# Kernel tuning notes

Hardware: AMD Instinct MI355X
Metric: run time of the kernel (lower is better)

The kernel has to match this reference:

```python
import jax, jax.numpy as jnp
import numpy as np

DECAY = 0.99
K = 8192
DIM = 512


def setup_inputs() -> dict:
    key = jax.random.key(0)
    k1, k2 = jax.random.split(key)
    z = jax.random.normal(k1, (8, 4096, DIM), dtype=jnp.float32)
    codebook = jax.random.normal(k2, (K, DIM), dtype=jnp.float32) * 0.02
    ema_count = jnp.zeros((K,), dtype=jnp.float32)
    ema_sum = jnp.zeros((K, DIM), dtype=jnp.float32)
    return {"z": z, "codebook": codebook, "ema_count": ema_count, "ema_sum": ema_sum}


def reference(z, codebook, ema_count, ema_sum):
    B, S, D = z.shape
    k = codebook.shape[0]
    z_flat = z.reshape(-1, D)  # [N, D]

    # squared euclidean distance: ||z||^2 + ||c||^2 - 2 z.c  -> [N, k]
    z2 = jnp.sum(z_flat * z_flat, axis=1, keepdims=True)
    c2 = jnp.sum(codebook * codebook, axis=1)
    logits = z_flat @ codebook.T
    dist = z2 + c2[None, :] - 2.0 * logits
    indices = jnp.argmin(dist, axis=1)  # [N]

    z_q = codebook[indices].reshape(z.shape)
    z_q_st = z + jax.lax.stop_gradient(z_q - z)  # straight-through

    loss_commit = jnp.mean((jax.lax.stop_gradient(z_q) - z) ** 2)
    loss_embed = jnp.mean((z_q - jax.lax.stop_gradient(z)) ** 2)

    # usage histogram (bincount), normalized
    ones = jnp.ones_like(indices, dtype=z.dtype)
    counts = jax.ops.segment_sum(ones, indices, num_segments=k)
    total = jnp.sum(counts)
    usage = jnp.where(total > 0, counts / total, counts)

    # EMA update (training-mode buffer update, all detached)
    zf = jax.lax.stop_gradient(z_flat)
    sums = jax.ops.segment_sum(zf, indices, num_segments=k)  # index_add
    new_ema_count = ema_count * DECAY + counts * (1.0 - DECAY)
    new_ema_sum = ema_sum * DECAY + sums * (1.0 - DECAY)
    denom = jnp.clip(new_ema_count[:, None], 1.0, None)
    new_codebook = new_ema_sum / denom

    return (z_q_st, indices.reshape(B, S), loss_commit, loss_embed, usage,
            new_codebook, new_ema_count, new_ema_sum)
```

## Files before the change

kernel.cpp:

```cpp
#include <hip/hip_runtime.h>


#define DIMC 512
#define NTOK 32768
#define KCB  8192

#define OFF_IDX   16777216UL
#define OFF_LC    16809984UL
#define OFF_LE    16809985UL
#define OFF_USAGE 16809986UL
#define OFF_NCB   16818178UL
#define OFF_NEC   21012482UL
#define OFF_NES   21020674UL

typedef unsigned short u16;
typedef unsigned int u32;
typedef __attribute__((ext_vector_type(8))) short short8;
typedef __attribute__((ext_vector_type(8))) u16 ushort8;
typedef __attribute__((ext_vector_type(4))) float f32x4;

__device__ __forceinline__ u16 f2bf(float x) {
  u32 u = __float_as_uint(x);
  return (u16)((u + 0x7fffu + ((u >> 16) & 1u)) >> 16);
}
__device__ __forceinline__ float bf2f(u16 h) { return __uint_as_float(((u32)h) << 16); }

#define GLL16(g, l) __builtin_amdgcn_global_load_lds( \
    (const __attribute__((address_space(1))) u32*)(g), \
    (__attribute__((address_space(3))) u32*)(l), 16, 0, 0)

__global__ __launch_bounds__(256)
void conv_norms(const float* __restrict__ z, const float* __restrict__ cb,
                u16* __restrict__ zh, u16* __restrict__ zl,
                u16* __restrict__ ch, u16* __restrict__ cl,
                float* __restrict__ z2, float* __restrict__ c2) {
  const int gid = blockIdx.x * 256 + threadIdx.x;
  const int lane = threadIdx.x & 63;
  int t = gid >> 6;
  const int g = gid & 63;
  const float* src; u16 *dh, *dl; float* nrm;
  if (t < NTOK) { src = z; dh = zh; dl = zl; nrm = z2; }
  else { t -= NTOK; src = cb; dh = ch; dl = cl; nrm = c2; }
  const float* p = src + (size_t)t * DIMC + g * 8;
  float4 v0 = *(const float4*)p;
  float4 v1 = *(const float4*)(p + 4);
  float in[8] = {v0.x, v0.y, v0.z, v0.w, v1.x, v1.y, v1.z, v1.w};
  ushort8 h, l;
  float ss = 0.f;
#pragma unroll
  for (int j = 0; j < 8; ++j) {
    ss += in[j] * in[j];
    u16 hb = f2bf(in[j]);
    h[j] = hb;
    l[j] = f2bf(in[j] - bf2f(hb));
  }
  const int mt = t >> 7, r = t & 127, ks = g >> 2, s = g & 3;
  const int sp = s ^ ((r >> 1) & 3);
  const size_t base = ((((size_t)mt * 16 + ks) * 128 + r) * 4 + sp) * 8;
  *(ushort8*)&dh[base] = h;
  *(ushort8*)&dl[base] = l;
#pragma unroll
  for (int off = 32; off; off >>= 1) ss += __shfl_down(ss, off);
  if (lane == 0) nrm[t] = ss;
}

__global__ __launch_bounds__(256)
void initkeys(unsigned long long* __restrict__ keys, double* __restrict__ loss) {
  const int i = blockIdx.x * 256 + threadIdx.x;
  keys[i] = 0xFFFFFFFFFFFFFFFFull;
  if (i == 0) *loss = 0.0;
}

__global__ __launch_bounds__(256)
void argmin_kernel(const u16* __restrict__ zh, const u16* __restrict__ zl,
                   const u16* __restrict__ ch, const u16* __restrict__ cl,
                   const float* __restrict__ z2, const float* __restrict__ c2,
                   unsigned long long* __restrict__ keys) {
  __shared__ __align__(16) char lds[32768];
  const int tid = threadIdx.x;
  const int mt = blockIdx.x, nt = blockIdx.y;
  const int lane = tid & 63;
  const int wid = tid >> 6;
  const int wr = wid >> 1, wn = wid & 1;
  const int lg = lane >> 4, lr = lane & 15;

  f32x4 acc[4][4];
#pragma unroll
  for (int m = 0; m < 4; ++m)
#pragma unroll
    for (int n = 0; n < 4; ++n) acc[m][n] = (f32x4)(0.f);

  const size_t abase = (size_t)mt * (16 * 4096);
  const size_t bbase = (size_t)nt * (16 * 4096);
  char* const la  = lds;
  char* const lal = lds + 8192;
  char* const lb  = lds + 16384;
  char* const lbl = lds + 24576;
  const int wlds = wid * 1024;
  const int goff = tid * 8;

  int aoff[4], boff[4];
#pragma unroll
  for (int m = 0; m < 4; ++m) {
    const int r = wr * 64 + m * 16 + lr;
    aoff[m] = r * 64 + ((lg ^ ((r >> 1) & 3)) * 16);
  }
#pragma unroll
  for (int n = 0; n < 4; ++n) {
    const int c = wn * 64 + n * 16 + lr;
    boff[n] = c * 64 + ((lg ^ ((c >> 1) & 3)) * 16);
  }

  for (int ks = 0; ks < 16; ++ks) {
    const size_t ao = abase + ks * 4096;
    const size_t bo = bbase + ks * 4096;
    __syncthreads();
    GLL16(zh + ao + goff,        la  + wlds);
    GLL16(zh + ao + 2048 + goff, la  + 4096 + wlds);
    GLL16(zl + ao + goff,        lal + wlds);
    GLL16(zl + ao + 2048 + goff, lal + 4096 + wlds);
    GLL16(ch + bo + goff,        lb  + wlds);
    GLL16(ch + bo + 2048 + goff, lb  + 4096 + wlds);
    GLL16(cl + bo + goff,        lbl + wlds);
    GLL16(cl + bo + 2048 + goff, lbl + 4096 + wlds);
    __syncthreads();
    short8 ah[4], alo[4], bh[4], blo[4];
#pragma unroll
    for (int m = 0; m < 4; ++m) {
      ah[m]  = *(const short8*)(la  + aoff[m]);
      alo[m] = *(const short8*)(lal + aoff[m]);
    }
#pragma unroll
    for (int n = 0; n < 4; ++n) {
      bh[n]  = *(const short8*)(lb  + boff[n]);
      blo[n] = *(const short8*)(lbl + boff[n]);
    }
#pragma unroll
    for (int m = 0; m < 4; ++m)
#pragma unroll
      for (int n = 0; n < 4; ++n) {
        acc[m][n] = __builtin_amdgcn_mfma_f32_16x16x32_bf16(alo[m], bh[n],  acc[m][n], 0, 0, 0);
        acc[m][n] = __builtin_amdgcn_mfma_f32_16x16x32_bf16(ah[m],  blo[n], acc[m][n], 0, 0, 0);
        acc[m][n] = __builtin_amdgcn_mfma_f32_16x16x32_bf16(ah[m],  bh[n],  acc[m][n], 0, 0, 0);
      }
  }

  const int row0 = mt * 128 + wr * 64;
  const int col0 = nt * 128 + wn * 64;
  float z2r[4][4];
#pragma unroll
  for (int m = 0; m < 4; ++m)
#pragma unroll
    for (int q = 0; q < 4; ++q)
      z2r[m][q] = z2[row0 + m * 16 + lg * 4 + q];
  float bv[4][4]; int bi[4][4];
#pragma unroll
  for (int m = 0; m < 4; ++m)
#pragma unroll
    for (int q = 0; q < 4; ++q) { bv[m][q] = 3.4e38f; bi[m][q] = 0x7fffffff; }
#pragma unroll
  for (int n = 0; n < 4; ++n) {
    const int cc = col0 + n * 16 + lr;
    const float c2v = c2[cc];
#pragma unroll
    for (int m = 0; m < 4; ++m)
#pragma unroll
      for (int q = 0; q < 4; ++q) {
        const float d = fmaf(-2.f, acc[m][n][q], z2r[m][q] + c2v);
        if (d < bv[m][q]) { bv[m][q] = d; bi[m][q] = cc; }
      }
  }
#pragma unroll
  for (int off = 1; off < 16; off <<= 1) {
#pragma unroll
    for (int m = 0; m < 4; ++m)
#pragma unroll
      for (int q = 0; q < 4; ++q) {
        const float ov = __shfl_xor(bv[m][q], off);
        const int oi = __shfl_xor(bi[m][q], off);
        if (ov < bv[m][q] || (ov == bv[m][q] && oi < bi[m][q])) { bv[m][q] = ov; bi[m][q] = oi; }
      }
  }
  if (lr == 0) {
#pragma unroll
    for (int m = 0; m < 4; ++m)
#pragma unroll
      for (int q = 0; q < 4; ++q) {
        const int token = row0 + m * 16 + lg * 4 + q;
        const unsigned long long pk =
            ((unsigned long long)__float_as_uint(bv[m][q]) << 32) | (u32)bi[m][q];
        atomicMin(&keys[token], pk);
      }
  }
}

__global__ __launch_bounds__(256)
void zero_kernel(float* __restrict__ usage_counts, float* __restrict__ sums) {
  const int gid = blockIdx.x * 256 + threadIdx.x;
  float2 zz; zz.x = 0.f; zz.y = 0.f;
  ((float2*)sums)[gid] = zz;
  ((float2*)sums)[gid + 1048576] = zz;
  if (gid < KCB) usage_counts[gid] = 0.f;
}

__global__ __launch_bounds__(128)
void gather_kernel(const float* __restrict__ z, const float* __restrict__ cb,
                   const unsigned long long* __restrict__ keys,
                   float* __restrict__ out, float* __restrict__ counts_acc,
                   float* __restrict__ sums_acc, double* __restrict__ loss_acc) {
  const int token = blockIdx.x;
  const int tid = threadIdx.x;
  const int idx = (int)(u32)(keys[token] & 0xFFFFFFFFull);
  if (tid == 0) {
    out[OFF_IDX + token] = (float)idx;
    unsafeAtomicAdd(&counts_acc[idx], 1.0f);
  }
  const float4 zv = *(const float4*)&z[(size_t)token * DIMC + tid * 4];
  const float4 cv = *(const float4*)&cb[(size_t)idx * DIMC + tid * 4];
  float4 o;
  o.x = zv.x + (cv.x - zv.x);
  o.y = zv.y + (cv.y - zv.y);
  o.z = zv.z + (cv.z - zv.z);
  o.w = zv.w + (cv.w - zv.w);
  *(float4*)&out[(size_t)token * DIMC + tid * 4] = o;
  const float ex = cv.x - zv.x, ey = cv.y - zv.y, ez = cv.z - zv.z, ew = cv.w - zv.w;
  float lsum = ex * ex; lsum += ey * ey; lsum += ez * ez; lsum += ew * ew;
  float* sp = &sums_acc[(size_t)idx * DIMC + tid * 4];
  unsafeAtomicAdd(sp + 0, zv.x);
  unsafeAtomicAdd(sp + 1, zv.y);
  unsafeAtomicAdd(sp + 2, zv.z);
  unsafeAtomicAdd(sp + 3, zv.w);
#pragma unroll
  for (int off = 32; off; off >>= 1) lsum += __shfl_down(lsum, off);
  if ((tid & 63) == 0) unsafeAtomicAdd(loss_acc, (double)lsum);
}

__global__ __launch_bounds__(256)
void finalize_mat(const float* __restrict__ ema_sum_in, const float* __restrict__ ema_cnt_in,
                  const float* __restrict__ counts_raw, float* __restrict__ nes,
                  float* __restrict__ ncb) {
  const int i2 = blockIdx.x * 256 + threadIdx.x;
  const size_t base = (size_t)i2 * 2;
  const int k = i2 >> 8;
  const float c = counts_raw[k];
  const float ncnt = ema_cnt_in[k] * 0.99f + c * 0.01f;
  const float denom = fmaxf(ncnt, 1.0f);
  float2 s = *(float2*)&nes[base];
  float2 e = *(const float2*)&ema_sum_in[base];
  float2 ns; ns.x = e.x * 0.99f + s.x * 0.01f; ns.y = e.y * 0.99f + s.y * 0.01f;
  *(float2*)&nes[base] = ns;
  float2 q; q.x = ns.x / denom; q.y = ns.y / denom;
  *(float2*)&ncb[base] = q;
}

__global__ __launch_bounds__(256)
void finalize_small(const float* __restrict__ ema_cnt_in, float* __restrict__ usage_io,
                    float* __restrict__ new_cnt_out, const double* __restrict__ loss_acc,
                    float* __restrict__ loss_out) {
  const int k = blockIdx.x * 256 + threadIdx.x;
  const float c = usage_io[k];
  usage_io[k] = c / 32768.0f;
  new_cnt_out[k] = ema_cnt_in[k] * 0.99f + c * 0.01f;
  if (k == 0) {
    const float l = (float)(*loss_acc / 16777216.0);
    loss_out[0] = l;
    loss_out[1] = l;
  }
}

extern "C" void kernel_launch(void* const* d_in, const int* in_sizes, int n_in,
                              void* d_out, int out_size, void* d_ws, size_t ws_size,
                              hipStream_t stream) {
  const float* z       = (const float*)d_in[0];
  const float* cb      = (const float*)d_in[1];
  const float* ema_cnt = (const float*)d_in[2];
  const float* ema_sum = (const float*)d_in[3];
  float* out = (float*)d_out;
  char* ws = (char*)d_ws;

  u16* zh = (u16*)out;
  u16* zl = (u16*)(out + 8388608);
  u16* ch = (u16*)(out + OFF_NCB + 2);
  u16* cl = (u16*)(out + OFF_NES + 2);
  unsigned long long* keys = (unsigned long long*)ws;
  float*  z2   = (float*)(ws + 262144);
  float*  c2   = (float*)(ws + 393216);
  double* loss = (double*)(ws + 425984);

  conv_norms<<<10240, 256, 0, stream>>>(z, cb, zh, zl, ch, cl, z2, c2);
  initkeys<<<128, 256, 0, stream>>>(keys, loss);
  argmin_kernel<<<dim3(256, 64), 256, 0, stream>>>(zh, zl, ch, cl, z2, c2, keys);
  zero_kernel<<<4096, 256, 0, stream>>>(out + OFF_USAGE, out + OFF_NES);
  gather_kernel<<<NTOK, 128, 0, stream>>>(z, cb, keys, out,
                                          out + OFF_USAGE, out + OFF_NES, loss);
  finalize_mat<<<8192, 256, 0, stream>>>(ema_sum, ema_cnt, out + OFF_USAGE,
                                         out + OFF_NES, out + OFF_NCB);
  finalize_small<<<32, 256, 0, stream>>>(ema_cnt, out + OFF_USAGE, out + OFF_NEC,
                                         loss, out + OFF_LC);
}
```

Baseline: 2.000 ms.

## Replace atomic segment-sum with counting sort and per-code gather reduction

After: 1.971 ms. About the same (-1.5%).

```diff
diff --git a/kernel.cpp b/kernel.cpp
--- a/kernel.cpp
+++ b/kernel.cpp
@@ -65,9 +65,11 @@
 }
 
 __global__ __launch_bounds__(256)
-void initkeys(unsigned long long* __restrict__ keys, double* __restrict__ loss) {
+void init_kernel(unsigned long long* __restrict__ keys, int* __restrict__ counts,
+                 double* __restrict__ loss) {
   const int i = blockIdx.x * 256 + threadIdx.x;
   keys[i] = 0xFFFFFFFFFFFFFFFFull;
+  if (i < KCB) counts[i] = 0;
   if (i == 0) *loss = 0.0;
 }
 
@@ -195,26 +197,61 @@
 }
 
 __global__ __launch_bounds__(256)
-void zero_kernel(float* __restrict__ usage_counts, float* __restrict__ sums) {
-  const int gid = blockIdx.x * 256 + threadIdx.x;
-  float2 zz; zz.x = 0.f; zz.y = 0.f;
-  ((float2*)sums)[gid] = zz;
-  ((float2*)sums)[gid + 1048576] = zz;
-  if (gid < KCB) usage_counts[gid] = 0.f;
+void hist_kernel(const unsigned long long* __restrict__ keys,
+                 int* __restrict__ counts, float* __restrict__ idx_out) {
+  const int t = blockIdx.x * 256 + threadIdx.x;
+  const int idx = (int)(u32)(keys[t] & 0xFFFFFFFFull);
+  idx_out[t] = (float)idx;
+  atomicAdd(&counts[idx], 1);
+}
+
+__global__ __launch_bounds__(1024)
+void scan_kernel(const int* __restrict__ counts, int* __restrict__ offsets,
+                 const float* __restrict__ ema_cnt, float* __restrict__ usage_out,
+                 float* __restrict__ nec_out) {
+  __shared__ int wsum[16];
+  const int t = threadIdx.x;
+  const int lane = t & 63, w = t >> 6;
+  int v[8]; int tot = 0;
+#pragma unroll
+  for (int j = 0; j < 8; ++j) { v[j] = counts[t * 8 + j]; tot += v[j]; }
+  int s = tot;
+#pragma unroll
+  for (int off = 1; off < 64; off <<= 1) {
+    const int u = __shfl_up(s, off);
+    if (lane >= off) s += u;
+  }
+  if (lane == 63) wsum[w] = s;
+  __syncthreads();
+  if (t == 0) { int a = 0; for (int i = 0; i < 16; ++i) { int b = wsum[i]; wsum[i] = a; a += b; } }
+  __syncthreads();
+  int base = wsum[w] + (s - tot);
+#pragma unroll
+  for (int j = 0; j < 8; ++j) {
+    const int k = t * 8 + j;
+    offsets[k] = base;
+    usage_out[k] = (float)v[j] * (1.0f / 32768.0f);
+    nec_out[k] = ema_cnt[k] * 0.99f + (float)v[j] * 0.01f;
+    base += v[j];
+  }
+}
+
+__global__ __launch_bounds__(256)
+void scatter_kernel(const unsigned long long* __restrict__ keys,
+                    int* __restrict__ offsets, int* __restrict__ list) {
+  const int t = blockIdx.x * 256 + threadIdx.x;
+  const int idx = (int)(u32)(keys[t] & 0xFFFFFFFFull);
+  const int pos = atomicAdd(&offsets[idx], 1);
+  list[pos] = t;
 }
 
 __global__ __launch_bounds__(128)
-void gather_kernel(const float* __restrict__ z, const float* __restrict__ cb,
-                   const unsigned long long* __restrict__ keys,
-                   float* __restrict__ out, float* __restrict__ counts_acc,
-                   float* __restrict__ sums_acc, double* __restrict__ loss_acc) {
+void zq_loss_kernel(const float* __restrict__ z, const float* __restrict__ cb,
+                    const unsigned long long* __restrict__ keys,
+                    float* __restrict__ out, double* __restrict__ loss_acc) {
   const int token = blockIdx.x;
   const int tid = threadIdx.x;
   const int idx = (int)(u32)(keys[token] & 0xFFFFFFFFull);
-  if (tid == 0) {
-    out[OFF_IDX + token] = (float)idx;
-    unsafeAtomicAdd(&counts_acc[idx], 1.0f);
-  }
   const float4 zv = *(const float4*)&z[(size_t)token * DIMC + tid * 4];
   const float4 cv = *(const float4*)&cb[(size_t)idx * DIMC + tid * 4];
   float4 o;
@@ -225,47 +262,47 @@
   *(float4*)&out[(size_t)token * DIMC + tid * 4] = o;
   const float ex = cv.x - zv.x, ey = cv.y - zv.y, ez = cv.z - zv.z, ew = cv.w - zv.w;
   float lsum = ex * ex; lsum += ey * ey; lsum += ez * ez; lsum += ew * ew;
-  float* sp = &sums_acc[(size_t)idx * DIMC + tid * 4];
-  unsafeAtomicAdd(sp + 0, zv.x);
-  unsafeAtomicAdd(sp + 1, zv.y);
-  unsafeAtomicAdd(sp + 2, zv.z);
-  unsafeAtomicAdd(sp + 3, zv.w);
 #pragma unroll
   for (int off = 32; off; off >>= 1) lsum += __shfl_down(lsum, off);
   if ((tid & 63) == 0) unsafeAtomicAdd(loss_acc, (double)lsum);
 }
 
-__global__ __launch_bounds__(256)
-void finalize_mat(const float* __restrict__ ema_sum_in, const float* __restrict__ ema_cnt_in,
-                  const float* __restrict__ counts_raw, float* __restrict__ nes,
-                  float* __restrict__ ncb) {
-  const int i2 = blockIdx.x * 256 + threadIdx.x;
-  const size_t base = (size_t)i2 * 2;
-  const int k = i2 >> 8;
-  const float c = counts_raw[k];
-  const float ncnt = ema_cnt_in[k] * 0.99f + c * 0.01f;
-  const float denom = fmaxf(ncnt, 1.0f);
-  float2 s = *(float2*)&nes[base];
-  float2 e = *(const float2*)&ema_sum_in[base];
-  float2 ns; ns.x = e.x * 0.99f + s.x * 0.01f; ns.y = e.y * 0.99f + s.y * 0.01f;
-  *(float2*)&nes[base] = ns;
-  float2 q; q.x = ns.x / denom; q.y = ns.y / denom;
-  *(float2*)&ncb[base] = q;
-}
-
-__global__ __launch_bounds__(256)
-void finalize_small(const float* __restrict__ ema_cnt_in, float* __restrict__ usage_io,
-                    float* __restrict__ new_cnt_out, const double* __restrict__ loss_acc,
-                    float* __restrict__ loss_out) {
-  const int k = blockIdx.x * 256 + threadIdx.x;
-  const float c = usage_io[k];
-  usage_io[k] = c / 32768.0f;
-  new_cnt_out[k] = ema_cnt_in[k] * 0.99f + c * 0.01f;
-  if (k == 0) {
+__global__ __launch_bounds__(128)
+void persum_kernel(const float* __restrict__ z, const float* __restrict__ ema_sum,
+                   const float* __restrict__ ema_cnt,
+                   const int* __restrict__ counts, const int* __restrict__ ends,
+                   const int* __restrict__ list,
+                   float* __restrict__ nes, float* __restrict__ ncb,
+                   const double* __restrict__ loss_acc, float* __restrict__ loss_out) {
+  const int k = blockIdx.x;
+  const int tid = threadIdx.x;
+  if (k == 0 && tid == 0) {
     const float l = (float)(*loss_acc / 16777216.0);
     loss_out[0] = l;
     loss_out[1] = l;
   }
+  const int cnt = counts[k];
+  const int start = ends[k] - cnt;
+  float4 s; s.x = s.y = s.z = s.w = 0.f;
+  for (int i = 0; i < cnt; ++i) {
+    const int tok = list[start + i];
+    const float4 zv = *(const float4*)&z[(size_t)tok * DIMC + tid * 4];
+    s.x += zv.x; s.y += zv.y; s.z += zv.z; s.w += zv.w;
+  }
+  const float ncnt = ema_cnt[k] * 0.99f + (float)cnt * 0.01f;
+  const float denom = fmaxf(ncnt, 1.0f);
+  const size_t base = (size_t)k * DIMC + tid * 4;
+  const float4 e = *(const float4*)&ema_sum[base];
+  float2 n0, n1;
+  n0.x = e.x * 0.99f + s.x * 0.01f; n0.y = e.y * 0.99f + s.y * 0.01f;
+  n1.x = e.z * 0.99f + s.z * 0.01f; n1.y = e.w * 0.99f + s.w * 0.01f;
+  *(float2*)&nes[base] = n0;
+  *(float2*)&nes[base + 2] = n1;
+  float2 q0, q1;
+  q0.x = n0.x / denom; q0.y = n0.y / denom;
+  q1.x = n1.x / denom; q1.y = n1.y / denom;
+  *(float2*)&ncb[base] = q0;
+  *(float2*)&ncb[base + 2] = q1;
 }
 
 extern "C" void kernel_launch(void* const* d_in, const int* in_sizes, int n_in,
@@ -283,18 +320,22 @@
   u16* ch = (u16*)(out + OFF_NCB + 2);
   u16* cl = (u16*)(out + OFF_NES + 2);
   unsigned long long* keys = (unsigned long long*)ws;
-  float*  z2   = (float*)(ws + 262144);
-  float*  c2   = (float*)(ws + 393216);
-  double* loss = (double*)(ws + 425984);
+  float* z2      = (float*)(ws + 262144);
+  float* c2      = (float*)(ws + 393216);
+  double* loss   = (double*)(ws + 425984);
+  int* counts    = (int*)(ws + 426240);
+  int* offsets   = (int*)(ws + 459008);
+  int* list      = (int*)(ws + 491776);
 
   conv_norms<<<10240, 256, 0, stream>>>(z, cb, zh, zl, ch, cl, z2, c2);
-  initkeys<<<128, 256, 0, stream>>>(keys, loss);
+  init_kernel<<<128, 256, 0, stream>>>(keys, counts, loss);
   argmin_kernel<<<dim3(256, 64), 256, 0, stream>>>(zh, zl, ch, cl, z2, c2, keys);
-  zero_kernel<<<4096, 256, 0, stream>>>(out + OFF_USAGE, out + OFF_NES);
-  gather_kernel<<<NTOK, 128, 0, stream>>>(z, cb, keys, out,
-                                          out + OFF_USAGE, out + OFF_NES, loss);
-  finalize_mat<<<8192, 256, 0, stream>>>(ema_sum, ema_cnt, out + OFF_USAGE,
-                                         out + OFF_NES, out + OFF_NCB);
-  finalize_small<<<32, 256, 0, stream>>>(ema_cnt, out + OFF_USAGE, out + OFF_NEC,
+  hist_kernel<<<128, 256, 0, stream>>>(keys, counts, out + OFF_IDX);
+  scan_kernel<<<1, 1024, 0, stream>>>(counts, offsets, ema_cnt,
+                                      out + OFF_USAGE, out + OFF_NEC);
+  scatter_kernel<<<128, 256, 0, stream>>>(keys, offsets, list);
+  zq_loss_kernel<<<NTOK, 128, 0, stream>>>(z, cb, keys, out, loss);
+  persum_kernel<<<KCB, 128, 0, stream>>>(z, ema_sum, ema_cnt, counts, offsets, list,
+                                         out + OFF_NES, out + OFF_NCB,
                                          loss, out + OFF_LC);
 }
```
